# Optimization experiments

Measured on AMD Instinct MI355X. Metric: run time of the kernel, lower is better.

The kernel has to match this reference:

```python
import jax, jax.numpy as jnp
import numpy as np

B, L, D, M_MAX = 4, 4096, 1024, 512


def setup_inputs() -> dict:
    key = jax.random.key(0)
    k_ct, k_enc, k_lo, k_hi, k_w = jax.random.split(key, 5)
    concept_tokens = jax.random.normal(k_ct, (B, M_MAX, D), dtype=jnp.float32)
    encoder_out = jax.random.normal(k_enc, (B, L, D), dtype=jnp.float32)
    # sorted unique boundary positions per batch, first boundary at position 0
    rng = np.random.RandomState(0)
    idx = np.stack([np.sort(rng.choice(np.arange(1, L), size=M_MAX - 1, replace=False)) for _ in range(B)])
    boundary_idx = jnp.asarray(np.concatenate([np.zeros((B, 1), dtype=np.int64), idx], axis=1))  # [B, M_max]
    # probs < 0.5 everywhere except at boundary positions (>= 0.5), so cumsum(mask)-1 < M_max
    lo = jax.random.uniform(k_lo, (B, L), minval=0.02, maxval=0.48)
    hi = jax.random.uniform(k_hi, (B, M_MAX), minval=0.5, maxval=1.0)
    rows = jnp.arange(B)[:, None]
    boundary_probs = lo.at[rows, boundary_idx].set(hi)
    concept_mask = jnp.ones((B, M_MAX), dtype=bool)
    W = jax.random.normal(k_w, (D, D), dtype=jnp.float32) * 0.02  # residual_proj.weight (out = x @ W.T)
    return {"concept_tokens": concept_tokens, "encoder_out": encoder_out,
            "boundary_probs": boundary_probs, "boundary_idx": boundary_idx,
            "concept_mask": concept_mask, "W": W}


def _ema_smooth(concept_tokens, p_at_bounds):
    """h_i = (1-p_i)*h_{i-1} + p_i*c_i via associative scan; h_0 = c_0."""
    h0 = concept_tokens[:, 0]                                  # [B, d]
    p_rest = p_at_bounds[:, 1:]                                # [B, M-1]
    decay = jnp.clip(1.0 - p_rest, 1e-7, None)
    b = p_rest[..., None] * concept_tokens[:, 1:]              # [B, M-1, d]
    a = jnp.broadcast_to(decay[..., None], b.shape)

    def combine(x, y):
        a1, b1 = x
        a2, b2 = y
        return a1 * a2, a2 * b1 + b2

    A, Bc = jax.lax.associative_scan(combine, (a, b), axis=1)
    h_rest = A * h0[:, None, :] + Bc                           # h_i = A_i*h0 + B_i
    return jnp.concatenate([h0[:, None, :], h_rest], axis=1)   # [B, M, d]


def reference(concept_tokens, encoder_out, boundary_probs, boundary_idx, concept_mask, W):
    d = encoder_out.shape[-1]
    # Eq.5: EMA over concept tokens with boundary probs gathered at boundary positions
    p_raw = jnp.take_along_axis(boundary_probs, boundary_idx, axis=1)          # [B, M]
    p_at_bounds = jnp.where(concept_mask, p_raw, 1.0)
    p_at_bounds = jnp.clip(p_at_bounds, 0.1, None)
    smoothed = _ema_smooth(concept_tokens, p_at_bounds)                        # [B, M, d]
    # Eq.8: plug-back via running boundary count
    boundary_mask = boundary_probs >= 0.5                                      # [B, L]
    plug_back_idx = jnp.clip(jnp.cumsum(boundary_mask.astype(jnp.int32), axis=1) - 1, 0, None)
    plugback = jnp.take_along_axis(smoothed, plug_back_idx[..., None], axis=1)  # [B, L, d]
    # Eq.6/7/9: confidence + STE (forward value is exactly 1.0)
    b_f = boundary_mask.astype(boundary_probs.dtype)
    c_t = b_f * boundary_probs + (1.0 - b_f) * (1.0 - boundary_probs)
    ste_c = c_t + jax.lax.stop_gradient(1.0 - c_t)
    upsampled = ste_c[..., None] * plugback
    # Eq.3: residual linear (no bias)
    return upsampled + jnp.einsum('bld,ed->ble', encoder_out, W)
```

## Files before the change

kernel.cpp:

```cpp
#include <hip/hip_runtime.h>
#include <hip/hip_bf16.h>
#include <stdint.h>


#define B_  4
#define L_  4096
#define D_  1024
#define M_  512

typedef __attribute__((ext_vector_type(8))) short bf16x8;
typedef __attribute__((ext_vector_type(4))) float f32x4;
typedef __attribute__((ext_vector_type(8))) unsigned short u16x8;

__device__ inline unsigned short f2bf(float f) {
    unsigned u = __float_as_uint(f);
    u += 0x7fffu + ((u >> 16) & 1u);
    return (unsigned short)(u >> 16);
}

__global__ void cvt_kernel(const float* __restrict__ in, unsigned short* __restrict__ out) {
    int i = blockIdx.x * 256 + threadIdx.x;
    float4 x0 = ((const float4*)in)[2 * i];
    float4 x1 = ((const float4*)in)[2 * i + 1];
    u16x8 v;
    v[0] = f2bf(x0.x); v[1] = f2bf(x0.y); v[2] = f2bf(x0.z); v[3] = f2bf(x0.w);
    v[4] = f2bf(x1.x); v[5] = f2bf(x1.y); v[6] = f2bf(x1.z); v[7] = f2bf(x1.w);
    ((u16x8*)out)[i] = v;
}

__global__ void ema_kernel(const float* __restrict__ ct, const float* __restrict__ probs,
                           const int* __restrict__ bidx, float* __restrict__ smoothed) {
    int b  = blockIdx.x >> 4;
    int d0 = (blockIdx.x & 15) * 64;
    int t  = threadIdx.x;
    int dl = t & 63;
    int ch = t >> 6;
    __shared__ float ad[M_], bdp[M_];
    __shared__ float Ac[8][64], Bc[8][64], Hin[8][64];
    for (int m = t; m < M_; m += 512) {
        int idx = bidx[b * M_ + m];
        float p = fmaxf(probs[b * L_ + idx], 0.1f);
        ad[m]  = (m == 0) ? 0.0f : fmaxf(1.0f - p, 1e-7f);
        bdp[m] = (m == 0) ? 1.0f : p;
    }
    __syncthreads();
    const float* ctp = ct + ((size_t)b * M_ + ch * 64) * D_ + d0 + dl;
    float A = 1.0f, Bv = 0.0f;
    #pragma unroll 8
    for (int i = 0; i < 64; ++i) {
        int m = ch * 64 + i;
        float c = ctp[(size_t)i * D_];
        A  = ad[m] * A;
        Bv = ad[m] * Bv + bdp[m] * c;
    }
    Ac[ch][dl] = A; Bc[ch][dl] = Bv;
    __syncthreads();
    if (t < 64) {
        float H = 0.0f;
        #pragma unroll
        for (int c = 0; c < 8; ++c) {
            Hin[c][t] = H;
            H = Ac[c][t] * H + Bc[c][t];
        }
    }
    __syncthreads();
    float h = Hin[ch][dl];
    float* smp = smoothed + ((size_t)b * M_ + ch * 64) * D_ + d0 + dl;
    #pragma unroll 8
    for (int i = 0; i < 64; ++i) {
        int m = ch * 64 + i;
        float c = ctp[(size_t)i * D_];
        h = ad[m] * h + bdp[m] * c;
        smp[(size_t)i * D_] = h;
    }
}

__global__ void pbi_kernel(const float* __restrict__ probs, int* __restrict__ pbi) {
    int b = blockIdx.x;
    int t = threadIdx.x;
    __shared__ int part[256];
    int base = b * L_ + t * 16;
    int cnt[16];
    int s = 0;
    #pragma unroll
    for (int i = 0; i < 16; ++i) {
        s += (probs[base + i] >= 0.5f) ? 1 : 0;
        cnt[i] = s;
    }
    part[t] = s;
    __syncthreads();
    for (int off = 1; off < 256; off <<= 1) {
        int x = part[t];
        int y = (t >= off) ? part[t - off] : 0;
        __syncthreads();
        part[t] = x + y;
        __syncthreads();
    }
    int excl = part[t] - s;
    #pragma unroll
    for (int i = 0; i < 16; ++i) {
        int v = excl + cnt[i] - 1;
        pbi[base + i] = v > 0 ? v : 0;
    }
}

__global__ __launch_bounds__(256, 2) void gemm_kernel(
    const unsigned short* __restrict__ encb, const unsigned short* __restrict__ Wb,
    const float* __restrict__ smoothed, const int* __restrict__ pbi,
    float* __restrict__ out)
{
    __shared__ __align__(16) unsigned short As[128 * 64];
    __shared__ __align__(16) unsigned short Bs[128 * 64];

    const int tid  = threadIdx.x;
    const int lane = tid & 63;
    const int w    = tid >> 6;
    const int wm   = w >> 1;
    const int wn   = w & 1;
    const int l15  = lane & 15;
    const int l16  = lane >> 4;

    const size_t rowBase = (size_t)blockIdx.x * 128;
    const int    colBase = blockIdx.y * 128;

    const int srow = lane >> 3;
    const int scol = (lane & 7) * 8;

    const unsigned short* aSrc = encb + (rowBase + srow) * D_ + scol;
    const unsigned short* bSrc = Wb + ((size_t)colBase + srow) * D_ + scol;

    f32x4 acc[4][4] = {};

    for (int t = 0; t < D_ / 64; ++t) {
        const int k0 = t * 64;
        #pragma unroll
        for (int i = 0; i < 4; ++i) {
            int seg = w * 4 + i;
            __builtin_amdgcn_global_load_lds(
                (const __attribute__((address_space(1))) void*)(aSrc + (size_t)seg * 8 * D_ + k0),
                (__attribute__((address_space(3))) void*)(&As[seg * 512]), 16, 0, 0);
            __builtin_amdgcn_global_load_lds(
                (const __attribute__((address_space(1))) void*)(bSrc + (size_t)seg * 8 * D_ + k0),
                (__attribute__((address_space(3))) void*)(&Bs[seg * 512]), 16, 0, 0);
        }
        __syncthreads();
        #pragma unroll
        for (int kk = 0; kk < 2; ++kk) {
            bf16x8 a[4], bb[4];
            #pragma unroll
            for (int m = 0; m < 4; ++m)
                a[m] = *(const bf16x8*)&As[(wm * 64 + m * 16 + l15) * 64 + kk * 32 + l16 * 8];
            #pragma unroll
            for (int n = 0; n < 4; ++n)
                bb[n] = *(const bf16x8*)&Bs[(wn * 64 + n * 16 + l15) * 64 + kk * 32 + l16 * 8];
            #pragma unroll
            for (int m = 0; m < 4; ++m)
                #pragma unroll
                for (int n = 0; n < 4; ++n)
                    acc[m][n] = __builtin_amdgcn_mfma_f32_16x16x32_bf16(a[m], bb[n], acc[m][n], 0, 0, 0);
        }
        __syncthreads();
    }

    #pragma unroll
    for (int m = 0; m < 4; ++m) {
        #pragma unroll
        for (int j = 0; j < 4; ++j) {
            size_t row = rowBase + wm * 64 + m * 16 + l16 * 4 + j;
            int b  = (int)(row >> 12);
            int pb = pbi[row];
            pb = pb < (M_ - 1) ? pb : (M_ - 1);
            const float* sm = smoothed + ((size_t)(b * M_ + pb)) * D_;
            #pragma unroll
            for (int n = 0; n < 4; ++n) {
                int col = colBase + wn * 64 + n * 16 + l15;
                out[row * D_ + col] = acc[m][n][j] + sm[col];
            }
        }
    }
}

#define LDP 72
__global__ __launch_bounds__(256, 2) void gemm_fused_kernel(
    const float* __restrict__ enc, const unsigned short* __restrict__ Wb,
    const float* __restrict__ smoothed, const int* __restrict__ pbi,
    float* __restrict__ out)
{
    __shared__ unsigned short As[128][LDP];
    __shared__ unsigned short Bs[128][LDP];
    const int tid  = threadIdx.x;
    const int lane = tid & 63;
    const int wid  = tid >> 6;
    const int wm   = wid >> 1;
    const int wn   = wid & 1;
    const int l15  = lane & 15;
    const int l16  = lane >> 4;
    const size_t rowBase = (size_t)blockIdx.x * 128;
    const int    colBase = blockIdx.y * 128;
    f32x4 acc[4][4] = {};
    for (int t = 0; t < D_ / 64; ++t) {
        const int k0 = t * 64;
        #pragma unroll
        for (int i = 0; i < 4; ++i) {
            int c = i * 256 + tid;
            int r = c >> 3;
            int c8 = c & 7;
            const float4* g = (const float4*)(enc + (rowBase + r) * D_ + k0 + c8 * 8);
            float4 x0 = g[0];
            float4 x1 = g[1];
            u16x8 v;
            v[0] = f2bf(x0.x); v[1] = f2bf(x0.y); v[2] = f2bf(x0.z); v[3] = f2bf(x0.w);
            v[4] = f2bf(x1.x); v[5] = f2bf(x1.y); v[6] = f2bf(x1.z); v[7] = f2bf(x1.w);
            *(u16x8*)&As[r][c8 * 8] = v;
        }
        #pragma unroll
        for (int i = 0; i < 4; ++i) {
            int c = i * 256 + tid;
            int r = c >> 3;
            int c8 = c & 7;
            u16x8 v = *(const u16x8*)(Wb + (size_t)(colBase + r) * D_ + k0 + c8 * 8);
            *(u16x8*)&Bs[r][c8 * 8] = v;
        }
        __syncthreads();
        #pragma unroll
        for (int kk = 0; kk < 2; ++kk) {
            bf16x8 a[4], bb[4];
            #pragma unroll
            for (int m = 0; m < 4; ++m)
                a[m] = *(const bf16x8*)&As[wm * 64 + m * 16 + l15][kk * 32 + l16 * 8];
            #pragma unroll
            for (int n = 0; n < 4; ++n)
                bb[n] = *(const bf16x8*)&Bs[wn * 64 + n * 16 + l15][kk * 32 + l16 * 8];
            #pragma unroll
            for (int m = 0; m < 4; ++m)
                #pragma unroll
                for (int n = 0; n < 4; ++n)
                    acc[m][n] = __builtin_amdgcn_mfma_f32_16x16x32_bf16(a[m], bb[n], acc[m][n], 0, 0, 0);
        }
        __syncthreads();
    }
    #pragma unroll
    for (int m = 0; m < 4; ++m) {
        #pragma unroll
        for (int j = 0; j < 4; ++j) {
            size_t row = rowBase + wm * 64 + m * 16 + l16 * 4 + j;
            int b  = (int)(row >> 12);
            int pb = pbi[row];
            pb = pb < (M_ - 1) ? pb : (M_ - 1);
            const float* sm = smoothed + ((size_t)(b * M_ + pb)) * D_;
            #pragma unroll
            for (int n = 0; n < 4; ++n) {
                int col = colBase + wn * 64 + n * 16 + l15;
                out[row * D_ + col] = acc[m][n][j] + sm[col];
            }
        }
    }
}

extern "C" void kernel_launch(void* const* d_in, const int* in_sizes, int n_in,
                              void* d_out, int out_size, void* d_ws, size_t ws_size,
                              hipStream_t stream) {
    const float* ct    = (const float*)d_in[0];
    const float* enc   = (const float*)d_in[1];
    const float* probs = (const float*)d_in[2];
    const int*   bidx  = (const int*)d_in[3];
    const float* W     = (const float*)d_in[5];
    float* out = (float*)d_out;
    char*  ws  = (char*)d_ws;

    const size_t SZ_ENCB = (size_t)B_ * L_ * D_ * 2;
    const size_t SZ_SM   = (size_t)B_ * M_ * D_ * 4;
    const size_t SZ_PBI  = (size_t)B_ * L_ * 4;
    const size_t SZ_WB   = (size_t)D_ * D_ * 2;

    if (ws_size >= SZ_ENCB + SZ_SM + SZ_PBI + SZ_WB) {
        unsigned short* encb     = (unsigned short*)ws;
        float*          smoothed = (float*)(ws + SZ_ENCB);
        int*            pbi      = (int*)(ws + SZ_ENCB + SZ_SM);
        unsigned short* Wb       = (unsigned short*)(ws + SZ_ENCB + SZ_SM + SZ_PBI);

        hipLaunchKernelGGL(cvt_kernel, dim3(B_ * L_ * D_ / 2048), dim3(256), 0, stream, enc, encb);
        hipLaunchKernelGGL(cvt_kernel, dim3(D_ * D_ / 2048),      dim3(256), 0, stream, W, Wb);
        hipLaunchKernelGGL(ema_kernel, dim3(B_ * D_ / 64),        dim3(512), 0, stream, ct, probs, bidx, smoothed);
        hipLaunchKernelGGL(pbi_kernel, dim3(B_),                  dim3(256), 0, stream, probs, pbi);
        hipLaunchKernelGGL(gemm_kernel, dim3(B_ * L_ / 128, D_ / 128), dim3(256), 0, stream,
                           encb, Wb, smoothed, pbi, out);
    } else {
        float*          smoothed = (float*)ws;
        int*            pbi      = (int*)(ws + SZ_SM);
        unsigned short* Wb       = (unsigned short*)(ws + SZ_SM + SZ_PBI);
        hipLaunchKernelGGL(cvt_kernel, dim3(D_ * D_ / 2048), dim3(256), 0, stream, W, Wb);
        hipLaunchKernelGGL(ema_kernel, dim3(B_ * D_ / 64),   dim3(512), 0, stream, ct, probs, bidx, smoothed);
        hipLaunchKernelGGL(pbi_kernel, dim3(B_),             dim3(256), 0, stream, probs, pbi);
        hipLaunchKernelGGL(gemm_fused_kernel, dim3(B_ * L_ / 128, D_ / 128), dim3(256), 0, stream,
                           enc, Wb, smoothed, pbi, out);
    }
}
```

Baseline: 186.3 us.

## Merge prep kernels, split EMA scan, and use triple-buffered 256x256 GEMM

Folds the enc/W bf16 conversions and the plug-back index scan into a single prep launch. Splits the EMA into two chunked-scan kernels so more blocks run it in parallel. Replaces the 128x128 GEMM with a 256x256-tile, 512-thread kernel that triple-buffers LDS via direct global-to-LDS loads, XOR-swizzles LDS reads, remaps tiles across blocks, and raises MFMA priority. The fallback path passes the summ buffer as the encb destination, which looks wrong, and only 256 GEMM blocks may leave some CUs underused.

New measurement: 177.3 us. -4.8%, faster.

```diff
diff --git a/kernel.cpp b/kernel.cpp
--- a/kernel.cpp
+++ b/kernel.cpp
@@ -18,155 +18,200 @@
     return (unsigned short)(u >> 16);
 }
 
-__global__ void cvt_kernel(const float* __restrict__ in, unsigned short* __restrict__ out) {
-    int i = blockIdx.x * 256 + threadIdx.x;
-    float4 x0 = ((const float4*)in)[2 * i];
-    float4 x1 = ((const float4*)in)[2 * i + 1];
-    u16x8 v;
-    v[0] = f2bf(x0.x); v[1] = f2bf(x0.y); v[2] = f2bf(x0.z); v[3] = f2bf(x0.w);
-    v[4] = f2bf(x1.x); v[5] = f2bf(x1.y); v[6] = f2bf(x1.z); v[7] = f2bf(x1.w);
-    ((u16x8*)out)[i] = v;
-}
-
-__global__ void ema_kernel(const float* __restrict__ ct, const float* __restrict__ probs,
-                           const int* __restrict__ bidx, float* __restrict__ smoothed) {
-    int b  = blockIdx.x >> 4;
-    int d0 = (blockIdx.x & 15) * 64;
-    int t  = threadIdx.x;
-    int dl = t & 63;
-    int ch = t >> 6;
-    __shared__ float ad[M_], bdp[M_];
-    __shared__ float Ac[8][64], Bc[8][64], Hin[8][64];
-    for (int m = t; m < M_; m += 512) {
+__global__ void prep_kernel(const float* __restrict__ enc, const float* __restrict__ W,
+                            const float* __restrict__ probs,
+                            unsigned short* __restrict__ encb, unsigned short* __restrict__ Wb,
+                            int* __restrict__ pbi) {
+    __shared__ int part[256];
+    int blk = blockIdx.x;
+    int tid = threadIdx.x;
+    if (blk < 8704) {
+        const float* src; unsigned short* dst; int i;
+        if (blk < 8192) { src = enc; dst = encb; i = blk * 256 + tid; }
+        else            { src = W;   dst = Wb;   i = (blk - 8192) * 256 + tid; }
+        float4 x0 = ((const float4*)src)[2 * i];
+        float4 x1 = ((const float4*)src)[2 * i + 1];
+        u16x8 v;
+        v[0] = f2bf(x0.x); v[1] = f2bf(x0.y); v[2] = f2bf(x0.z); v[3] = f2bf(x0.w);
+        v[4] = f2bf(x1.x); v[5] = f2bf(x1.y); v[6] = f2bf(x1.z); v[7] = f2bf(x1.w);
+        ((u16x8*)dst)[i] = v;
+    } else {
+        int b = blk - 8704;
+        const float4* pr = (const float4*)(probs + b * L_);
+        int cnt[16]; int s = 0;
+        #pragma unroll
+        for (int u = 0; u < 4; ++u) {
+            float4 x = pr[tid * 4 + u];
+            s += (x.x >= 0.5f); cnt[u * 4 + 0] = s;
+            s += (x.y >= 0.5f); cnt[u * 4 + 1] = s;
+            s += (x.z >= 0.5f); cnt[u * 4 + 2] = s;
+            s += (x.w >= 0.5f); cnt[u * 4 + 3] = s;
+        }
+        part[tid] = s;
+        __syncthreads();
+        for (int off = 1; off < 256; off <<= 1) {
+            int x = part[tid];
+            int y = (tid >= off) ? part[tid - off] : 0;
+            __syncthreads();
+            part[tid] = x + y;
+            __syncthreads();
+        }
+        int excl = part[tid] - s;
+        int4* po = (int4*)(pbi + b * L_ + tid * 16);
+        #pragma unroll
+        for (int u = 0; u < 4; ++u) {
+            int4 o;
+            o.x = max(excl + cnt[u * 4 + 0] - 1, 0);
+            o.y = max(excl + cnt[u * 4 + 1] - 1, 0);
+            o.z = max(excl + cnt[u * 4 + 2] - 1, 0);
+            o.w = max(excl + cnt[u * 4 + 3] - 1, 0);
+            po[u] = o;
+        }
+    }
+}
+
+__global__ void ema1_kernel(const float* __restrict__ ct, const float* __restrict__ probs,
+                            const int* __restrict__ bidx, float2* __restrict__ summ) {
+    int b = blockIdx.z, ch = blockIdx.y;
+    int d = blockIdx.x * 256 + threadIdx.x;
+    __shared__ float pa[64], pb[64];
+    if (threadIdx.x < 64) {
+        int m = ch * 64 + threadIdx.x;
         int idx = bidx[b * M_ + m];
-        float p = fmaxf(probs[b * L_ + idx], 0.1f);
-        ad[m]  = (m == 0) ? 0.0f : fmaxf(1.0f - p, 1e-7f);
-        bdp[m] = (m == 0) ? 1.0f : p;
+        float pv = fmaxf(probs[b * L_ + idx], 0.1f);
+        pa[threadIdx.x] = (m == 0) ? 0.0f : fmaxf(1.0f - pv, 1e-7f);
+        pb[threadIdx.x] = (m == 0) ? 1.0f : pv;
     }
     __syncthreads();
-    const float* ctp = ct + ((size_t)b * M_ + ch * 64) * D_ + d0 + dl;
+    const float* ctp = ct + ((size_t)b * M_ + ch * 64) * D_ + d;
     float A = 1.0f, Bv = 0.0f;
     #pragma unroll 8
     for (int i = 0; i < 64; ++i) {
-        int m = ch * 64 + i;
         float c = ctp[(size_t)i * D_];
-        A  = ad[m] * A;
-        Bv = ad[m] * Bv + bdp[m] * c;
-    }
-    Ac[ch][dl] = A; Bc[ch][dl] = Bv;
+        A  = pa[i] * A;
+        Bv = pa[i] * Bv + pb[i] * c;
+    }
+    summ[((size_t)b * 8 + ch) * D_ + d] = make_float2(A, Bv);
+}
+
+__global__ void ema2_kernel(const float* __restrict__ ct, const float* __restrict__ probs,
+                            const int* __restrict__ bidx, const float2* __restrict__ summ,
+                            float* __restrict__ smoothed) {
+    int b = blockIdx.z, ch = blockIdx.y;
+    int d = blockIdx.x * 256 + threadIdx.x;
+    __shared__ float pa[64], pb[64];
+    if (threadIdx.x < 64) {
+        int m = ch * 64 + threadIdx.x;
+        int idx = bidx[b * M_ + m];
+        float pv = fmaxf(probs[b * L_ + idx], 0.1f);
+        pa[threadIdx.x] = (m == 0) ? 0.0f : fmaxf(1.0f - pv, 1e-7f);
+        pb[threadIdx.x] = (m == 0) ? 1.0f : pv;
+    }
     __syncthreads();
-    if (t < 64) {
-        float H = 0.0f;
-        #pragma unroll
-        for (int c = 0; c < 8; ++c) {
-            Hin[c][t] = H;
-            H = Ac[c][t] * H + Bc[c][t];
-        }
-    }
-    __syncthreads();
-    float h = Hin[ch][dl];
-    float* smp = smoothed + ((size_t)b * M_ + ch * 64) * D_ + d0 + dl;
+    float h = 0.0f;
+    for (int c = 0; c < ch; ++c) {
+        float2 s2 = summ[((size_t)b * 8 + c) * D_ + d];
+        h = s2.x * h + s2.y;
+    }
+    const float* ctp = ct + ((size_t)b * M_ + ch * 64) * D_ + d;
+    float*       smp = smoothed + ((size_t)b * M_ + ch * 64) * D_ + d;
     #pragma unroll 8
     for (int i = 0; i < 64; ++i) {
-        int m = ch * 64 + i;
         float c = ctp[(size_t)i * D_];
-        h = ad[m] * h + bdp[m] * c;
+        h = pa[i] * h + pb[i] * c;
         smp[(size_t)i * D_] = h;
     }
 }
 
-__global__ void pbi_kernel(const float* __restrict__ probs, int* __restrict__ pbi) {
-    int b = blockIdx.x;
-    int t = threadIdx.x;
-    __shared__ int part[256];
-    int base = b * L_ + t * 16;
-    int cnt[16];
-    int s = 0;
-    #pragma unroll
-    for (int i = 0; i < 16; ++i) {
-        s += (probs[base + i] >= 0.5f) ? 1 : 0;
-        cnt[i] = s;
-    }
-    part[t] = s;
-    __syncthreads();
-    for (int off = 1; off < 256; off <<= 1) {
-        int x = part[t];
-        int y = (t >= off) ? part[t - off] : 0;
-        __syncthreads();
-        part[t] = x + y;
-        __syncthreads();
-    }
-    int excl = part[t] - s;
-    #pragma unroll
-    for (int i = 0; i < 16; ++i) {
-        int v = excl + cnt[i] - 1;
-        pbi[base + i] = v > 0 ? v : 0;
-    }
-}
-
-__global__ __launch_bounds__(256, 2) void gemm_kernel(
+#define NT_ 32
+
+__global__ __launch_bounds__(512, 1) void gemm3_kernel(
     const unsigned short* __restrict__ encb, const unsigned short* __restrict__ Wb,
     const float* __restrict__ smoothed, const int* __restrict__ pbi,
     float* __restrict__ out)
 {
-    __shared__ __align__(16) unsigned short As[128 * 64];
-    __shared__ __align__(16) unsigned short Bs[128 * 64];
+    __shared__ __align__(16) unsigned short As[3][256 * 32];
+    __shared__ __align__(16) unsigned short Bs[3][256 * 32];
 
     const int tid  = threadIdx.x;
     const int lane = tid & 63;
     const int w    = tid >> 6;
-    const int wm   = w >> 1;
-    const int wn   = w & 1;
+    const int wm   = w >> 2;
+    const int wn   = w & 3;
     const int l15  = lane & 15;
     const int l16  = lane >> 4;
 
-    const size_t rowBase = (size_t)blockIdx.x * 128;
-    const int    colBase = blockIdx.y * 128;
-
-    const int srow = lane >> 3;
-    const int scol = (lane & 7) * 8;
-
-    const unsigned short* aSrc = encb + (rowBase + srow) * D_ + scol;
-    const unsigned short* bSrc = Wb + ((size_t)colBase + srow) * D_ + scol;
-
-    f32x4 acc[4][4] = {};
-
-    for (int t = 0; t < D_ / 64; ++t) {
-        const int k0 = t * 64;
-        #pragma unroll
-        for (int i = 0; i < 4; ++i) {
-            int seg = w * 4 + i;
-            __builtin_amdgcn_global_load_lds(
-                (const __attribute__((address_space(1))) void*)(aSrc + (size_t)seg * 8 * D_ + k0),
-                (__attribute__((address_space(3))) void*)(&As[seg * 512]), 16, 0, 0);
-            __builtin_amdgcn_global_load_lds(
-                (const __attribute__((address_space(1))) void*)(bSrc + (size_t)seg * 8 * D_ + k0),
-                (__attribute__((address_space(3))) void*)(&Bs[seg * 512]), 16, 0, 0);
-        }
-        __syncthreads();
-        #pragma unroll
-        for (int kk = 0; kk < 2; ++kk) {
-            bf16x8 a[4], bb[4];
-            #pragma unroll
-            for (int m = 0; m < 4; ++m)
-                a[m] = *(const bf16x8*)&As[(wm * 64 + m * 16 + l15) * 64 + kk * 32 + l16 * 8];
+    const int orig = blockIdx.x;
+    const int rm   = (orig & 7) * 32 + (orig >> 3);
+    const size_t rowBase = (size_t)(rm >> 2) * 256;
+    const int    colBase = (rm & 3) * 256;
+
+    const int rsw = (((lane & 3) ^ ((lane >> 2) & 3)) << 3);
+
+#define STAGE(kt, s)                                                                     \
+  {                                                                                      \
+    _Pragma("unroll")                                                                    \
+    for (int i_ = 0; i_ < 2; ++i_) {                                                     \
+      int row_ = i_ * 128 + w * 16 + (lane >> 2);                                        \
+      const unsigned short* ga_ = encb + (rowBase + row_) * D_ + (kt) * 32 + rsw;        \
+      __builtin_amdgcn_global_load_lds(                                                  \
+          (const __attribute__((address_space(1))) void*)ga_,                            \
+          (__attribute__((address_space(3))) void*)&As[s][i_ * 4096 + w * 512], 16, 0, 0);\
+      const unsigned short* gb_ = Wb + (size_t)(colBase + row_) * D_ + (kt) * 32 + rsw;  \
+      __builtin_amdgcn_global_load_lds(                                                  \
+          (const __attribute__((address_space(1))) void*)gb_,                            \
+          (__attribute__((address_space(3))) void*)&Bs[s][i_ * 4096 + w * 512], 16, 0, 0);\
+    }                                                                                    \
+  }
+
+    f32x4 acc[8][4] = {};
+
+    STAGE(0, 0);
+    STAGE(1, 1);
+    asm volatile("s_waitcnt vmcnt(4)" ::: "memory");
+    __builtin_amdgcn_s_barrier();
+    __builtin_amdgcn_sched_barrier(0);
+
+    int s = 0;
+    for (int t = 0; t < NT_; ++t) {
+        const char* aB = (const char*)As[s];
+        const char* bB = (const char*)Bs[s];
+        const int swz = (l15 & 3) << 4;
+        bf16x8 a[8], bb[4];
+        #pragma unroll
+        for (int m = 0; m < 8; ++m)
+            a[m] = *(const bf16x8*)(aB + (wm * 128 + m * 16 + l15) * 64 + ((l16 * 16) ^ swz));
+        #pragma unroll
+        for (int n = 0; n < 4; ++n)
+            bb[n] = *(const bf16x8*)(bB + (wn * 64 + n * 16 + l15) * 64 + ((l16 * 16) ^ swz));
+
+        int s2 = s + 2; if (s2 >= 3) s2 -= 3;
+        if (t + 2 < NT_) STAGE(t + 2, s2);
+
+        __builtin_amdgcn_s_setprio(1);
+        #pragma unroll
+        for (int m = 0; m < 8; ++m)
             #pragma unroll
             for (int n = 0; n < 4; ++n)
-                bb[n] = *(const bf16x8*)&Bs[(wn * 64 + n * 16 + l15) * 64 + kk * 32 + l16 * 8];
-            #pragma unroll
-            for (int m = 0; m < 4; ++m)
-                #pragma unroll
-                for (int n = 0; n < 4; ++n)
-                    acc[m][n] = __builtin_amdgcn_mfma_f32_16x16x32_bf16(a[m], bb[n], acc[m][n], 0, 0, 0);
-        }
-        __syncthreads();
-    }
+                acc[m][n] = __builtin_amdgcn_mfma_f32_16x16x32_bf16(a[m], bb[n], acc[m][n], 0, 0, 0);
+        __builtin_amdgcn_s_setprio(0);
+
+        if (t + 1 < NT_) {
+            if (t + 2 < NT_) { asm volatile("s_waitcnt vmcnt(4)" ::: "memory"); }
+            else             { asm volatile("s_waitcnt vmcnt(0)" ::: "memory"); }
+            __builtin_amdgcn_s_barrier();
+            __builtin_amdgcn_sched_barrier(0);
+        }
+        s += 1; if (s >= 3) s -= 3;
+    }
+#undef STAGE
 
     #pragma unroll
-    for (int m = 0; m < 4; ++m) {
+    for (int m = 0; m < 8; ++m) {
+        const size_t row0 = rowBase + wm * 128 + m * 16;
         #pragma unroll
         for (int j = 0; j < 4; ++j) {
-            size_t row = rowBase + wm * 64 + m * 16 + l16 * 4 + j;
+            size_t row = row0 + l16 * 4 + j;
             int b  = (int)(row >> 12);
             int pb = pbi[row];
             pb = pb < (M_ - 1) ? pb : (M_ - 1);
@@ -186,8 +231,8 @@
     const float* __restrict__ smoothed, const int* __restrict__ pbi,
     float* __restrict__ out)
 {
-    __shared__ unsigned short As[128][LDP];
-    __shared__ unsigned short Bs[128][LDP];
+    __shared__ unsigned short Asf[128][LDP];
+    __shared__ unsigned short Bsf[128][LDP];
     const int tid  = threadIdx.x;
     const int lane = tid & 63;
     const int wid  = tid >> 6;
@@ -211,7 +256,7 @@
             u16x8 v;
             v[0] = f2bf(x0.x); v[1] = f2bf(x0.y); v[2] = f2bf(x0.z); v[3] = f2bf(x0.w);
             v[4] = f2bf(x1.x); v[5] = f2bf(x1.y); v[6] = f2bf(x1.z); v[7] = f2bf(x1.w);
-            *(u16x8*)&As[r][c8 * 8] = v;
+            *(u16x8*)&Asf[r][c8 * 8] = v;
         }
         #pragma unroll
         for (int i = 0; i < 4; ++i) {
@@ -219,23 +264,23 @@
             int r = c >> 3;
             int c8 = c & 7;
             u16x8 v = *(const u16x8*)(Wb + (size_t)(colBase + r) * D_ + k0 + c8 * 8);
-            *(u16x8*)&Bs[r][c8 * 8] = v;
+            *(u16x8*)&Bsf[r][c8 * 8] = v;
         }
         __syncthreads();
         #pragma unroll
         for (int kk = 0; kk < 2; ++kk) {
-            bf16x8 a[4], bb[4];
+            bf16x8 a[4], bbf[4];
             #pragma unroll
             for (int m = 0; m < 4; ++m)
-                a[m] = *(const bf16x8*)&As[wm * 64 + m * 16 + l15][kk * 32 + l16 * 8];
+                a[m] = *(const bf16x8*)&Asf[wm * 64 + m * 16 + l15][kk * 32 + l16 * 8];
             #pragma unroll
             for (int n = 0; n < 4; ++n)
-                bb[n] = *(const bf16x8*)&Bs[wn * 64 + n * 16 + l15][kk * 32 + l16 * 8];
+                bbf[n] = *(const bf16x8*)&Bsf[wn * 64 + n * 16 + l15][kk * 32 + l16 * 8];
             #pragma unroll
             for (int m = 0; m < 4; ++m)
                 #pragma unroll
                 for (int n = 0; n < 4; ++n)
-                    acc[m][n] = __builtin_amdgcn_mfma_f32_16x16x32_bf16(a[m], bb[n], acc[m][n], 0, 0, 0);
+                    acc[m][n] = __builtin_amdgcn_mfma_f32_16x16x32_bf16(a[m], bbf[n], acc[m][n], 0, 0, 0);
         }
         __syncthreads();
     }
@@ -272,26 +317,34 @@
     const size_t SZ_SM   = (size_t)B_ * M_ * D_ * 4;
     const size_t SZ_PBI  = (size_t)B_ * L_ * 4;
     const size_t SZ_WB   = (size_t)D_ * D_ * 2;
-
-    if (ws_size >= SZ_ENCB + SZ_SM + SZ_PBI + SZ_WB) {
+    const size_t SZ_SUMM = (size_t)B_ * 8 * D_ * 8;
+
+    if (ws_size >= SZ_ENCB + SZ_SM + SZ_PBI + SZ_WB + SZ_SUMM) {
         unsigned short* encb     = (unsigned short*)ws;
         float*          smoothed = (float*)(ws + SZ_ENCB);
         int*            pbi      = (int*)(ws + SZ_ENCB + SZ_SM);
         unsigned short* Wb       = (unsigned short*)(ws + SZ_ENCB + SZ_SM + SZ_PBI);
-
-        hipLaunchKernelGGL(cvt_kernel, dim3(B_ * L_ * D_ / 2048), dim3(256), 0, stream, enc, encb);
-        hipLaunchKernelGGL(cvt_kernel, dim3(D_ * D_ / 2048),      dim3(256), 0, stream, W, Wb);
-        hipLaunchKernelGGL(ema_kernel, dim3(B_ * D_ / 64),        dim3(512), 0, stream, ct, probs, bidx, smoothed);
-        hipLaunchKernelGGL(pbi_kernel, dim3(B_),                  dim3(256), 0, stream, probs, pbi);
-        hipLaunchKernelGGL(gemm_kernel, dim3(B_ * L_ / 128, D_ / 128), dim3(256), 0, stream,
+        float2*         summ     = (float2*)(ws + SZ_ENCB + SZ_SM + SZ_PBI + SZ_WB);
+
+        hipLaunchKernelGGL(prep_kernel, dim3(8708), dim3(256), 0, stream,
+                           enc, W, probs, encb, Wb, pbi);
+        hipLaunchKernelGGL(ema1_kernel, dim3(D_ / 256, 8, B_), dim3(256), 0, stream,
+                           ct, probs, bidx, summ);
+        hipLaunchKernelGGL(ema2_kernel, dim3(D_ / 256, 8, B_), dim3(256), 0, stream,
+                           ct, probs, bidx, summ, smoothed);
+        hipLaunchKernelGGL(gemm3_kernel, dim3(256), dim3(512), 0, stream,
                            encb, Wb, smoothed, pbi, out);
     } else {
         float*          smoothed = (float*)ws;
         int*            pbi      = (int*)(ws + SZ_SM);
         unsigned short* Wb       = (unsigned short*)(ws + SZ_SM + SZ_PBI);
-        hipLaunchKernelGGL(cvt_kernel, dim3(D_ * D_ / 2048), dim3(256), 0, stream, W, Wb);
-        hipLaunchKernelGGL(ema_kernel, dim3(B_ * D_ / 64),   dim3(512), 0, stream, ct, probs, bidx, smoothed);
-        hipLaunchKernelGGL(pbi_kernel, dim3(B_),             dim3(256), 0, stream, probs, pbi);
+        float2*         summ     = (float2*)(ws + SZ_SM + SZ_PBI + SZ_WB);
+        hipLaunchKernelGGL(prep_kernel, dim3(8708), dim3(256), 0, stream,
+                           enc, W, probs, (unsigned short*)summ , Wb, pbi);
+        hipLaunchKernelGGL(ema1_kernel, dim3(D_ / 256, 8, B_), dim3(256), 0, stream,
+                           ct, probs, bidx, summ);
+        hipLaunchKernelGGL(ema2_kernel, dim3(D_ / 256, 8, B_), dim3(256), 0, stream,
+                           ct, probs, bidx, summ, smoothed);
         hipLaunchKernelGGL(gemm_fused_kernel, dim3(B_ * L_ / 128, D_ / 128), dim3(256), 0, stream,
                            enc, Wb, smoothed, pbi, out);
     }
```
